# Kernel optimization log

Hardware: AMD Instinct MI355X
Metric: run time of the kernel (lower is better)

The kernel has to match this reference:

```python
import jax, jax.numpy as jnp
import numpy as np

N_INNER = 16
N_INPUT = 784
NET_DIM = 64
N_CAT = 256
NIP = 256


def fourier(x, coeff):
    # x: [N, in_features], coeff: [in_features, net_dim//2]
    xp = 2.0 * jnp.pi * (x @ coeff)
    # concat(cos, sin) then transpose -> [net_dim, N]
    return jnp.concatenate([jnp.cos(xp), jnp.sin(xp)], axis=-1).T


def setup_inputs() -> dict:
    key = jax.random.key(0)
    ks = jax.random.split(key, 8)
    s = 0.05  # conv weight scale (~kaiming-uniform magnitude)
    z = jax.random.normal(ks[0], (NIP,), jnp.float32)
    log_w = jax.random.normal(ks[1], (NIP,), jnp.float32)
    inner_coeff = jax.random.normal(ks[2], (2, NET_DIM // 2), jnp.float32)  # sigma=1.0
    inner_w1 = jax.random.normal(ks[3], (N_INNER * NET_DIM, NET_DIM), jnp.float32) * s
    inner_w2 = jax.random.normal(ks[4], (N_INNER, NET_DIM), jnp.float32) * s
    input_coeff = jax.random.normal(ks[5], (1, NET_DIM // 2), jnp.float32)
    input_w1 = jax.random.normal(ks[6], (N_INPUT * NET_DIM, NET_DIM), jnp.float32) * s
    input_w2 = jax.random.normal(ks[7], (N_INPUT, N_CAT, NET_DIM), jnp.float32) * s
    return {"z": z, "log_w": log_w, "inner_coeff": inner_coeff,
            "inner_w1": inner_w1, "inner_w2": inner_w2,
            "input_coeff": input_coeff, "input_w1": input_w1,
            "input_w2": input_w2, "n_chunks": 1}


def reference(z, log_w, inner_coeff, inner_w1, inner_w2, input_coeff, input_w1, input_w2, n_chunks):
    nip = z.shape[0]
    # all-pairs grid: [nip^2, 2] (repeat_interleave, repeat)
    z2d = jnp.stack([jnp.repeat(z, nip), jnp.tile(z, nip)], axis=-1)
    # inner net (quad mode forces first conv groups=1 -> dense matmul)
    ff = fourier(z2d, inner_coeff)                 # [net_dim, nip^2]
    h = jnp.tanh(inner_w1 @ ff)                    # [N_INNER*net_dim, nip^2]
    h = h.reshape(N_INNER, NET_DIM, nip * nip)
    logits = -jax.nn.softplus(jnp.einsum('gd,gdn->gn', inner_w2, h))
    logits = logits.reshape(N_INNER, nip, nip)
    log_inner = logits - jax.nn.logsumexp(logits + log_w, axis=-1, keepdims=True) + log_w
    inner_param = jnp.swapaxes(jnp.exp(log_inner), -1, -2)   # [N_INNER, nip, nip]
    # input net
    ffi = fourier(z[:, None], input_coeff)         # [net_dim, nip]
    hi = jnp.tanh(input_w1 @ ffi).reshape(N_INPUT, NET_DIM, nip)
    in_logits = jnp.einsum('gcd,gdn->gcn', input_w2, hi)     # [N_INPUT, N_CAT, nip]
    input_param = jax.nn.log_softmax(jnp.swapaxes(in_logits, 1, 2), axis=-1)  # [N_INPUT, nip, N_CAT]
    return inner_param, input_param
```

## Files before the change

kernel.cpp:

```cpp
#include <hip/hip_runtime.h>

typedef unsigned short ushort_t;
typedef float f32x4 __attribute__((ext_vector_type(4)));
typedef __bf16 bf16x8 __attribute__((ext_vector_type(8)));

#define PI2 6.283185307179586f

__device__ inline float bf2f(ushort_t u){
  union { unsigned int i; float f; } x; x.i = ((unsigned int)u) << 16; return x.f;
}
__device__ inline float fast_tanh(float x){
  float e = __expf(2.0f*x);
  return 1.0f - 2.0f/(e + 1.0f);
}

__global__ __launch_bounds__(256, 4) void inner_kernel(
    const float* __restrict__ z,
    const float* __restrict__ log_w,
    const float* __restrict__ icoef,
    const float* __restrict__ w1,
    const float* __restrict__ w2,
    float* __restrict__ out0)
{
  const int tx   = threadIdx.x;
  const int lane = tx & 63, wid = tx >> 6;
  const int i    = blockIdx.x >> 2;
  const int gq   = blockIdx.x & 3;

  __shared__ __bf16 sh_ffB[16 * 2 * 64 * 8];
  __shared__ float  sredw[4][256];
  __shared__ float  sred4[4];

  const float zi = z[i];
  const float zj = z[tx];
  const float lw = log_w[tx];

  {
    const int t = tx >> 4, n = tx & 15;
    #pragma unroll
    for (int q = 0; q < 4; q++){
      union { __bf16 h[8]; uint4 v; } pc, ps;
      #pragma unroll
      for (int ii = 0; ii < 8; ii++){
        int k = 8*q + ii;
        float xp = PI2 * (zi*icoef[k] + zj*icoef[32+k]);
        float sv, cv;
        __sincosf(xp, &sv, &cv);
        pc.h[ii] = (__bf16)cv;
        ps.h[ii] = (__bf16)sv;
      }
      ((uint4*)sh_ffB)[(t*2+0)*64 + 16*q + n] = pc.v;
      ((uint4*)sh_ffB)[(t*2+1)*64 + 16*q + n] = ps.v;
    }
  }
  __syncthreads();

  const int w = wid;
  #pragma unroll 1
  for (int gg = 0; gg < 4; gg++){
    const int g = gq*4 + gg;

    const float* Ar = w1 + (size_t)(g*64 + 16*w + (lane&15))*64 + (lane>>4)*8;
    bf16x8 A0, A1;
    #pragma unroll
    for (int ii = 0; ii < 8; ii++){
      A0[ii] = (__bf16)Ar[ii];
      A1[ii] = (__bf16)Ar[32+ii];
    }
    const float4 w2v = *(const float4*)(w2 + g*64 + 16*w + 4*(lane>>4));

    float part[16];
    #pragma unroll 4
    for (int t = 0; t < 16; t++){
      bf16x8 B0 = *(const bf16x8*)(sh_ffB + ((size_t)(t*2+0)*64 + lane)*8);
      bf16x8 B1 = *(const bf16x8*)(sh_ffB + ((size_t)(t*2+1)*64 + lane)*8);
      f32x4 acc = {0.f, 0.f, 0.f, 0.f};
      acc = __builtin_amdgcn_mfma_f32_16x16x32_bf16(A0, B0, acc, 0, 0, 0);
      acc = __builtin_amdgcn_mfma_f32_16x16x32_bf16(A1, B1, acc, 0, 0, 0);
      float p = 0.f;
      p = fmaf(w2v.x, fast_tanh(acc[0]), p);
      p = fmaf(w2v.y, fast_tanh(acc[1]), p);
      p = fmaf(w2v.z, fast_tanh(acc[2]), p);
      p = fmaf(w2v.w, fast_tanh(acc[3]), p);
      part[t] = p;
    }
    #pragma unroll
    for (int t = 0; t < 16; t++){
      float p = part[t];
      p += __shfl_xor(p, 16, 64);
      p += __shfl_xor(p, 32, 64);
      if ((lane >> 4) == 0) sredw[w][t*16 + lane] = p;
    }
    __syncthreads();

    float y = sredw[0][tx] + sredw[1][tx] + sredw[2][tx] + sredw[3][tx];
    float sp = fmaxf(y, 0.f) + __logf(1.f + __expf(-fabsf(y)));
    float tval = -sp + lw;
    float m = tval;
    #pragma unroll
    for (int o = 32; o > 0; o >>= 1) m = fmaxf(m, __shfl_xor(m, o, 64));
    if (lane == 0) sred4[wid] = m;
    __syncthreads();
    m = fmaxf(fmaxf(sred4[0], sred4[1]), fmaxf(sred4[2], sred4[3]));
    __syncthreads();
    float e = __expf(tval - m);
    float s = e;
    #pragma unroll
    for (int o = 32; o > 0; o >>= 1) s += __shfl_xor(s, o, 64);
    if (lane == 0) sred4[wid] = s;
    __syncthreads();
    s = sred4[0] + sred4[1] + sred4[2] + sred4[3];
    float lse = m + __logf(s);
    out0[(size_t)g*65536 + (size_t)tx*256 + i] = __expf(tval - lse);
    __syncthreads();
  }
}

__global__ __launch_bounds__(256, 3) void input_kernel(
    const float* __restrict__ z,
    const float* __restrict__ ipc,
    const float* __restrict__ w1,
    const float* __restrict__ w2,
    float* __restrict__ out1)
{
  const int tx   = threadIdx.x;
  const int lane = tx & 63, wid = tx >> 6;
  const int b    = blockIdx.x;
  const int xcd  = b & 7;
  const int s    = b >> 3;
  const int g    = xcd*98 + (s >> 2);
  const int nt   = s & 3;

  __shared__ __bf16 sh_fB[4 * 2 * 64 * 8];
  __shared__ __bf16 sh_hB[4 * 2 * 64 * 8];
  __shared__ ushort_t sh_lg[64 * 260];
  __shared__ float sm[4][64], ssv[4][64], slse[64];

  {
    const int n = tx & 63, q = tx >> 6;
    const int t = n >> 4, nn = n & 15;
    const float zn = z[nt*64 + n];
    union { __bf16 h[8]; uint4 v; } pc, ps;
    #pragma unroll
    for (int ii = 0; ii < 8; ii++){
      float xp = PI2 * zn * ipc[8*q + ii];
      float sv, cv;
      __sincosf(xp, &sv, &cv);
      pc.h[ii] = (__bf16)cv;
      ps.h[ii] = (__bf16)sv;
    }
    ((uint4*)sh_fB)[(t*2+0)*64 + 16*q + nn] = pc.v;
    ((uint4*)sh_fB)[(t*2+1)*64 + 16*q + nn] = ps.v;
  }
  __syncthreads();

  {
    const int w = wid;
    const float* Ar = w1 + (size_t)g*4096 + (size_t)(16*w + (lane&15))*64 + (lane>>4)*8;
    bf16x8 A0, A1;
    #pragma unroll
    for (int ii = 0; ii < 8; ii++){
      A0[ii] = (__bf16)Ar[ii];
      A1[ii] = (__bf16)Ar[32+ii];
    }
    const int q2 = lane >> 4, nn = lane & 15;
    const int dlt = w >> 1;
    #pragma unroll
    for (int t = 0; t < 4; t++){
      bf16x8 B0 = *(const bf16x8*)(sh_fB + ((size_t)(t*2+0)*64 + lane)*8);
      bf16x8 B1 = *(const bf16x8*)(sh_fB + ((size_t)(t*2+1)*64 + lane)*8);
      f32x4 acc = {0.f, 0.f, 0.f, 0.f};
      acc = __builtin_amdgcn_mfma_f32_16x16x32_bf16(A0, B0, acc, 0, 0, 0);
      acc = __builtin_amdgcn_mfma_f32_16x16x32_bf16(A1, B1, acc, 0, 0, 0);
      #pragma unroll
      for (int r = 0; r < 4; r++){
        int d  = 16*w + 4*q2 + r;
        int qB = (d & 31) >> 3, iB = d & 7;
        sh_hB[((size_t)(t*2+dlt)*64 + qB*16 + nn)*8 + iB] = (__bf16)fast_tanh(acc[r]);
      }
    }
  }
  __syncthreads();

  {
    const int w = wid;
    const float* w2g = w2 + (size_t)g*16384;
    #pragma unroll 1
    for (int cc = 0; cc < 4; cc++){
      const int ct = 4*w + cc;
      const float* Ar = w2g + (size_t)(16*ct + (lane&15))*64 + (lane>>4)*8;
      bf16x8 A0, A1;
      #pragma unroll
      for (int ii = 0; ii < 8; ii++){
        A0[ii] = (__bf16)Ar[ii];
        A1[ii] = (__bf16)Ar[32+ii];
      }
      #pragma unroll
      for (int t = 0; t < 4; t++){
        bf16x8 B0 = *(const bf16x8*)(sh_hB + ((size_t)(t*2+0)*64 + lane)*8);
        bf16x8 B1 = *(const bf16x8*)(sh_hB + ((size_t)(t*2+1)*64 + lane)*8);
        f32x4 acc = {0.f, 0.f, 0.f, 0.f};
        acc = __builtin_amdgcn_mfma_f32_16x16x32_bf16(A0, B0, acc, 0, 0, 0);
        acc = __builtin_amdgcn_mfma_f32_16x16x32_bf16(A1, B1, acc, 0, 0, 0);
        int c0 = 16*ct + 4*(lane>>4);
        int nn = 16*t + (lane&15);
        union { ushort_t u[4]; uint2 v; } pk;
        #pragma unroll
        for (int r = 0; r < 4; r++){
          union { float f; unsigned int i; } x; x.f = acc[r];
          unsigned int rr = x.i + 0x7fffu + ((x.i >> 16) & 1u);
          pk.u[r] = (ushort_t)(rr >> 16);
        }
        *(uint2*)(sh_lg + (size_t)nn*260 + c0) = pk.v;
      }
    }
  }
  __syncthreads();

  {
    const int n = tx & 63, cq = tx >> 6;
    const ushort_t* row = sh_lg + (size_t)n*260 + cq*64;
    float m = -3.0e38f;
    #pragma unroll 4
    for (int ci = 0; ci < 64; ci++) m = fmaxf(m, bf2f(row[ci]));
    float s = 0.f;
    #pragma unroll 4
    for (int ci = 0; ci < 64; ci++) s += __expf(bf2f(row[ci]) - m);
    sm[cq][n] = m; ssv[cq][n] = s;
  }
  __syncthreads();
  if (tx < 64){
    float M = fmaxf(fmaxf(sm[0][tx], sm[1][tx]), fmaxf(sm[2][tx], sm[3][tx]));
    float S = ssv[0][tx]*__expf(sm[0][tx]-M) + ssv[1][tx]*__expf(sm[1][tx]-M)
            + ssv[2][tx]*__expf(sm[2][tx]-M) + ssv[3][tx]*__expf(sm[3][tx]-M);
    slse[tx] = M + __logf(S);
  }
  __syncthreads();
  {
    size_t base = (size_t)g*65536 + (size_t)nt*64*256;
    #pragma unroll 1
    for (int rr = 0; rr < 64; rr++){
      out1[base + (size_t)rr*256 + tx] = bf2f(sh_lg[(size_t)rr*260 + tx]) - slse[rr];
    }
  }
}

extern "C" void kernel_launch(void* const* d_in, const int* in_sizes, int n_in,
                              void* d_out, int out_size, void* d_ws, size_t ws_size,
                              hipStream_t stream)
{
  const float* z     = (const float*)d_in[0];
  const float* lw    = (const float*)d_in[1];
  const float* icoef = (const float*)d_in[2];
  const float* iw1   = (const float*)d_in[3];
  const float* iw2   = (const float*)d_in[4];
  const float* ipc   = (const float*)d_in[5];
  const float* inw1  = (const float*)d_in[6];
  const float* inw2  = (const float*)d_in[7];

  float* out0 = (float*)d_out;
  float* out1 = out0 + (size_t)16*256*256;

  hipLaunchKernelGGL(inner_kernel, dim3(1024), dim3(256), 0, stream, z, lw, icoef, iw1, iw2, out0);
  hipLaunchKernelGGL(input_kernel, dim3(3136), dim3(256), 0, stream, z, ipc, inw1, inw2, out1);
}
```

Measured before the change: 358.1 us.

## Fuse inner and input kernels into one launch with register-resident logits

Merges the two kernels into one grid in which the first 256 blocks handle the inner net and the rest handle the input net. The inner path now computes Fourier features on the fly per tile, keeps all four weight tiles in registers, does a per-row softmax with a shared-memory buffer, and writes coalesced float4 stores. The input path keeps logits in fp32 registers rather than rounding them to bf16 in LDS, does the log-softmax through warp shuffles plus a small LDS reduction, and writes vectorized output. Weight loads are vectorized as float4. The aim is to remove a launch boundary, cut LDS traffic and uncoalesced stores, at the cost of higher register pressure.

```diff
diff --git a/kernel.cpp b/kernel.cpp
--- a/kernel.cpp
+++ b/kernel.cpp
@@ -5,242 +5,278 @@
 typedef __bf16 bf16x8 __attribute__((ext_vector_type(8)));
 
 #define PI2 6.283185307179586f
-
-__device__ inline float bf2f(ushort_t u){
-  union { unsigned int i; float f; } x; x.i = ((unsigned int)u) << 16; return x.f;
-}
+#define N_INNER_BLOCKS 256
+#define N_INPUT_BLOCKS 3136
+
 __device__ inline float fast_tanh(float x){
   float e = __expf(2.0f*x);
   return 1.0f - 2.0f/(e + 1.0f);
 }
 
-__global__ __launch_bounds__(256, 4) void inner_kernel(
+__global__ __launch_bounds__(256, 3) void fused_kernel(
     const float* __restrict__ z,
     const float* __restrict__ log_w,
     const float* __restrict__ icoef,
-    const float* __restrict__ w1,
-    const float* __restrict__ w2,
-    float* __restrict__ out0)
+    const float* __restrict__ iw1,
+    const float* __restrict__ iw2,
+    const float* __restrict__ ipc,
+    const float* __restrict__ nw1,
+    const float* __restrict__ nw2,
+    float* __restrict__ out0,
+    float* __restrict__ out1)
 {
+  __shared__ __align__(16) char smem[18688];
   const int tx   = threadIdx.x;
-  const int lane = tx & 63, wid = tx >> 6;
-  const int i    = blockIdx.x >> 2;
-  const int gq   = blockIdx.x & 3;
-
-  __shared__ __bf16 sh_ffB[16 * 2 * 64 * 8];
-  __shared__ float  sredw[4][256];
-  __shared__ float  sred4[4];
-
-  const float zi = z[i];
-  const float zj = z[tx];
-  const float lw = log_w[tx];
-
-  {
-    const int t = tx >> 4, n = tx & 15;
-    #pragma unroll
-    for (int q = 0; q < 4; q++){
+  const int lane = tx & 63, w = tx >> 6;
+  const int q    = lane >> 4, l15 = lane & 15;
+
+  if (blockIdx.x < N_INNER_BLOCKS){
+    const int ib = blockIdx.x;
+    const int g  = ib >> 4;
+    const int i0 = (ib & 15) << 4;
+
+    float* res = (float*)smem;
+    float* zz  = (float*)(smem + 16640);
+    float* lwv = (float*)(smem + 17664);
+
+    zz[tx]  = z[tx];
+    lwv[tx] = log_w[tx];
+    __syncthreads();
+
+    float cA[8], cB[8];
+    #pragma unroll
+    for (int ii = 0; ii < 8; ii++){
+      cA[ii] = PI2 * icoef[8*q + ii];
+      cB[ii] = PI2 * icoef[32 + 8*q + ii];
+    }
+
+    bf16x8 A0[4], A1[4];
+    #pragma unroll
+    for (int dt = 0; dt < 4; dt++){
+      const float* Ar = iw1 + (size_t)(g*64 + 16*dt + l15)*64 + 8*q;
+      f32x4 a0 = *(const f32x4*)Ar;
+      f32x4 a1 = *(const f32x4*)(Ar + 4);
+      f32x4 a2 = *(const f32x4*)(Ar + 32);
+      f32x4 a3 = *(const f32x4*)(Ar + 36);
+      #pragma unroll
+      for (int ii = 0; ii < 4; ii++){
+        A0[dt][ii]   = (__bf16)a0[ii];
+        A0[dt][4+ii] = (__bf16)a1[ii];
+        A1[dt][ii]   = (__bf16)a2[ii];
+        A1[dt][4+ii] = (__bf16)a3[ii];
+      }
+    }
+    f32x4 w2v[4];
+    #pragma unroll
+    for (int dt = 0; dt < 4; dt++)
+      w2v[dt] = *(const f32x4*)(iw2 + g*64 + 16*dt + 4*q);
+
+    #pragma unroll 1
+    for (int il = 0; il < 4; il++){
+      const int irow = 4*w + il;
+      const float zi = zz[i0 + irow];
+      float xA[8];
+      #pragma unroll
+      for (int ii = 0; ii < 8; ii++) xA[ii] = zi * cA[ii];
+
+      float m = -3.0e38f;
+      #pragma unroll 2
+      for (int jt = 0; jt < 16; jt++){
+        const float zj = zz[16*jt + l15];
+        bf16x8 B0, B1;
+        #pragma unroll
+        for (int ii = 0; ii < 8; ii++){
+          float sv, cv;
+          __sincosf(xA[ii] + zj*cB[ii], &sv, &cv);
+          B0[ii] = (__bf16)cv;
+          B1[ii] = (__bf16)sv;
+        }
+        float p = 0.f;
+        #pragma unroll
+        for (int dt = 0; dt < 4; dt++){
+          f32x4 acc = {0.f, 0.f, 0.f, 0.f};
+          acc = __builtin_amdgcn_mfma_f32_16x16x32_bf16(A0[dt], B0, acc, 0, 0, 0);
+          acc = __builtin_amdgcn_mfma_f32_16x16x32_bf16(A1[dt], B1, acc, 0, 0, 0);
+          p = fmaf(w2v[dt][0], fast_tanh(acc[0]), p);
+          p = fmaf(w2v[dt][1], fast_tanh(acc[1]), p);
+          p = fmaf(w2v[dt][2], fast_tanh(acc[2]), p);
+          p = fmaf(w2v[dt][3], fast_tanh(acc[3]), p);
+        }
+        p += __shfl_xor(p, 16, 64);
+        p += __shfl_xor(p, 32, 64);
+        float sp = fmaxf(p, 0.f) + __logf(1.f + __expf(-fabsf(p)));
+        float tval = -sp + lwv[16*jt + l15];
+        if (q == 0) res[irow*260 + 16*jt + l15] = tval;
+        m = fmaxf(m, tval);
+      }
+      #pragma unroll
+      for (int o = 1; o < 16; o <<= 1) m = fmaxf(m, __shfl_xor(m, o, 64));
+      float s = 0.f;
+      #pragma unroll
+      for (int jt = 0; jt < 16; jt++)
+        s += __expf(res[irow*260 + 16*jt + l15] - m);
+      #pragma unroll
+      for (int o = 1; o < 16; o <<= 1) s += __shfl_xor(s, o, 64);
+      const float lse = m + __logf(s);
+      if (q == 0){
+        #pragma unroll
+        for (int jt = 0; jt < 16; jt++){
+          const int idx = irow*260 + 16*jt + l15;
+          res[idx] = __expf(res[idx] - lse);
+        }
+      }
+    }
+    __syncthreads();
+    {
+      const int j2 = tx >> 2, c4 = tx & 3;
+      const size_t base = (size_t)g*65536 + (size_t)i0 + 4*c4;
+      #pragma unroll
+      for (int it2 = 0; it2 < 4; it2++){
+        const int j = 64*it2 + j2;
+        f32x4 v;
+        #pragma unroll
+        for (int rr = 0; rr < 4; rr++) v[rr] = res[(4*c4 + rr)*260 + j];
+        *(f32x4*)(out0 + base + (size_t)j*256) = v;
+      }
+    }
+  } else {
+    const int b   = blockIdx.x - N_INNER_BLOCKS;
+    const int xcd = b & 7;
+    const int s5  = b >> 3;
+    const int g   = xcd*98 + (s5 >> 2);
+    const int nt  = s5 & 3;
+
+    __bf16* fB   = (__bf16*)smem;
+    __bf16* hB   = (__bf16*)(smem + 8192);
+    float*  wred = (float*)(smem + 16384);
+    float*  sred = (float*)(smem + 17408);
+
+    {
+      const int n = tx & 63, qq = tx >> 6;
+      const int t = n >> 4, nn = n & 15;
+      const float zn = z[nt*64 + n];
       union { __bf16 h[8]; uint4 v; } pc, ps;
       #pragma unroll
       for (int ii = 0; ii < 8; ii++){
-        int k = 8*q + ii;
-        float xp = PI2 * (zi*icoef[k] + zj*icoef[32+k]);
         float sv, cv;
-        __sincosf(xp, &sv, &cv);
+        __sincosf(PI2 * zn * ipc[8*qq + ii], &sv, &cv);
         pc.h[ii] = (__bf16)cv;
         ps.h[ii] = (__bf16)sv;
       }
-      ((uint4*)sh_ffB)[(t*2+0)*64 + 16*q + n] = pc.v;
-      ((uint4*)sh_ffB)[(t*2+1)*64 + 16*q + n] = ps.v;
-    }
-  }
-  __syncthreads();
-
-  const int w = wid;
-  #pragma unroll 1
-  for (int gg = 0; gg < 4; gg++){
-    const int g = gq*4 + gg;
-
-    const float* Ar = w1 + (size_t)(g*64 + 16*w + (lane&15))*64 + (lane>>4)*8;
-    bf16x8 A0, A1;
-    #pragma unroll
-    for (int ii = 0; ii < 8; ii++){
-      A0[ii] = (__bf16)Ar[ii];
-      A1[ii] = (__bf16)Ar[32+ii];
-    }
-    const float4 w2v = *(const float4*)(w2 + g*64 + 16*w + 4*(lane>>4));
-
-    float part[16];
-    #pragma unroll 4
-    for (int t = 0; t < 16; t++){
-      bf16x8 B0 = *(const bf16x8*)(sh_ffB + ((size_t)(t*2+0)*64 + lane)*8);
-      bf16x8 B1 = *(const bf16x8*)(sh_ffB + ((size_t)(t*2+1)*64 + lane)*8);
-      f32x4 acc = {0.f, 0.f, 0.f, 0.f};
-      acc = __builtin_amdgcn_mfma_f32_16x16x32_bf16(A0, B0, acc, 0, 0, 0);
-      acc = __builtin_amdgcn_mfma_f32_16x16x32_bf16(A1, B1, acc, 0, 0, 0);
-      float p = 0.f;
-      p = fmaf(w2v.x, fast_tanh(acc[0]), p);
-      p = fmaf(w2v.y, fast_tanh(acc[1]), p);
-      p = fmaf(w2v.z, fast_tanh(acc[2]), p);
-      p = fmaf(w2v.w, fast_tanh(acc[3]), p);
-      part[t] = p;
-    }
-    #pragma unroll
-    for (int t = 0; t < 16; t++){
-      float p = part[t];
-      p += __shfl_xor(p, 16, 64);
-      p += __shfl_xor(p, 32, 64);
-      if ((lane >> 4) == 0) sredw[w][t*16 + lane] = p;
-    }
-    __syncthreads();
-
-    float y = sredw[0][tx] + sredw[1][tx] + sredw[2][tx] + sredw[3][tx];
-    float sp = fmaxf(y, 0.f) + __logf(1.f + __expf(-fabsf(y)));
-    float tval = -sp + lw;
-    float m = tval;
-    #pragma unroll
-    for (int o = 32; o > 0; o >>= 1) m = fmaxf(m, __shfl_xor(m, o, 64));
-    if (lane == 0) sred4[wid] = m;
-    __syncthreads();
-    m = fmaxf(fmaxf(sred4[0], sred4[1]), fmaxf(sred4[2], sred4[3]));
-    __syncthreads();
-    float e = __expf(tval - m);
-    float s = e;
-    #pragma unroll
-    for (int o = 32; o > 0; o >>= 1) s += __shfl_xor(s, o, 64);
-    if (lane == 0) sred4[wid] = s;
-    __syncthreads();
-    s = sred4[0] + sred4[1] + sred4[2] + sred4[3];
-    float lse = m + __logf(s);
-    out0[(size_t)g*65536 + (size_t)tx*256 + i] = __expf(tval - lse);
-    __syncthreads();
-  }
-}
-
-__global__ __launch_bounds__(256, 3) void input_kernel(
-    const float* __restrict__ z,
-    const float* __restrict__ ipc,
-    const float* __restrict__ w1,
-    const float* __restrict__ w2,
-    float* __restrict__ out1)
-{
-  const int tx   = threadIdx.x;
-  const int lane = tx & 63, wid = tx >> 6;
-  const int b    = blockIdx.x;
-  const int xcd  = b & 7;
-  const int s    = b >> 3;
-  const int g    = xcd*98 + (s >> 2);
-  const int nt   = s & 3;
-
-  __shared__ __bf16 sh_fB[4 * 2 * 64 * 8];
-  __shared__ __bf16 sh_hB[4 * 2 * 64 * 8];
-  __shared__ ushort_t sh_lg[64 * 260];
-  __shared__ float sm[4][64], ssv[4][64], slse[64];
-
-  {
-    const int n = tx & 63, q = tx >> 6;
-    const int t = n >> 4, nn = n & 15;
-    const float zn = z[nt*64 + n];
-    union { __bf16 h[8]; uint4 v; } pc, ps;
-    #pragma unroll
-    for (int ii = 0; ii < 8; ii++){
-      float xp = PI2 * zn * ipc[8*q + ii];
-      float sv, cv;
-      __sincosf(xp, &sv, &cv);
-      pc.h[ii] = (__bf16)cv;
-      ps.h[ii] = (__bf16)sv;
-    }
-    ((uint4*)sh_fB)[(t*2+0)*64 + 16*q + nn] = pc.v;
-    ((uint4*)sh_fB)[(t*2+1)*64 + 16*q + nn] = ps.v;
-  }
-  __syncthreads();
-
-  {
-    const int w = wid;
-    const float* Ar = w1 + (size_t)g*4096 + (size_t)(16*w + (lane&15))*64 + (lane>>4)*8;
-    bf16x8 A0, A1;
-    #pragma unroll
-    for (int ii = 0; ii < 8; ii++){
-      A0[ii] = (__bf16)Ar[ii];
-      A1[ii] = (__bf16)Ar[32+ii];
-    }
-    const int q2 = lane >> 4, nn = lane & 15;
-    const int dlt = w >> 1;
-    #pragma unroll
-    for (int t = 0; t < 4; t++){
-      bf16x8 B0 = *(const bf16x8*)(sh_fB + ((size_t)(t*2+0)*64 + lane)*8);
-      bf16x8 B1 = *(const bf16x8*)(sh_fB + ((size_t)(t*2+1)*64 + lane)*8);
-      f32x4 acc = {0.f, 0.f, 0.f, 0.f};
-      acc = __builtin_amdgcn_mfma_f32_16x16x32_bf16(A0, B0, acc, 0, 0, 0);
-      acc = __builtin_amdgcn_mfma_f32_16x16x32_bf16(A1, B1, acc, 0, 0, 0);
-      #pragma unroll
-      for (int r = 0; r < 4; r++){
-        int d  = 16*w + 4*q2 + r;
-        int qB = (d & 31) >> 3, iB = d & 7;
-        sh_hB[((size_t)(t*2+dlt)*64 + qB*16 + nn)*8 + iB] = (__bf16)fast_tanh(acc[r]);
-      }
-    }
-  }
-  __syncthreads();
-
-  {
-    const int w = wid;
-    const float* w2g = w2 + (size_t)g*16384;
-    #pragma unroll 1
-    for (int cc = 0; cc < 4; cc++){
-      const int ct = 4*w + cc;
-      const float* Ar = w2g + (size_t)(16*ct + (lane&15))*64 + (lane>>4)*8;
+      ((uint4*)fB)[(t*2+0)*64 + 16*qq + nn] = pc.v;
+      ((uint4*)fB)[(t*2+1)*64 + 16*qq + nn] = ps.v;
+    }
+    __syncthreads();
+
+    {
+      const float* Ar = nw1 + (size_t)g*4096 + (size_t)(16*w + l15)*64 + 8*q;
+      f32x4 a0 = *(const f32x4*)Ar;
+      f32x4 a1 = *(const f32x4*)(Ar + 4);
+      f32x4 a2 = *(const f32x4*)(Ar + 32);
+      f32x4 a3 = *(const f32x4*)(Ar + 36);
       bf16x8 A0, A1;
       #pragma unroll
-      for (int ii = 0; ii < 8; ii++){
-        A0[ii] = (__bf16)Ar[ii];
-        A1[ii] = (__bf16)Ar[32+ii];
-      }
+      for (int ii = 0; ii < 4; ii++){
+        A0[ii] = (__bf16)a0[ii];  A0[4+ii] = (__bf16)a1[ii];
+        A1[ii] = (__bf16)a2[ii];  A1[4+ii] = (__bf16)a3[ii];
+      }
+      const int dlt = w >> 1;
+      const int qB  = 2*(w & 1) + (q >> 1);
+      const int iB0 = 4*(q & 1);
       #pragma unroll
       for (int t = 0; t < 4; t++){
-        bf16x8 B0 = *(const bf16x8*)(sh_hB + ((size_t)(t*2+0)*64 + lane)*8);
-        bf16x8 B1 = *(const bf16x8*)(sh_hB + ((size_t)(t*2+1)*64 + lane)*8);
+        bf16x8 B0 = *(const bf16x8*)(fB + ((t*2+0)*64 + lane)*8);
+        bf16x8 B1 = *(const bf16x8*)(fB + ((t*2+1)*64 + lane)*8);
         f32x4 acc = {0.f, 0.f, 0.f, 0.f};
         acc = __builtin_amdgcn_mfma_f32_16x16x32_bf16(A0, B0, acc, 0, 0, 0);
         acc = __builtin_amdgcn_mfma_f32_16x16x32_bf16(A1, B1, acc, 0, 0, 0);
-        int c0 = 16*ct + 4*(lane>>4);
-        int nn = 16*t + (lane&15);
-        union { ushort_t u[4]; uint2 v; } pk;
-        #pragma unroll
-        for (int r = 0; r < 4; r++){
-          union { float f; unsigned int i; } x; x.f = acc[r];
-          unsigned int rr = x.i + 0x7fffu + ((x.i >> 16) & 1u);
-          pk.u[r] = (ushort_t)(rr >> 16);
-        }
-        *(uint2*)(sh_lg + (size_t)nn*260 + c0) = pk.v;
-      }
-    }
-  }
-  __syncthreads();
-
-  {
-    const int n = tx & 63, cq = tx >> 6;
-    const ushort_t* row = sh_lg + (size_t)n*260 + cq*64;
-    float m = -3.0e38f;
-    #pragma unroll 4
-    for (int ci = 0; ci < 64; ci++) m = fmaxf(m, bf2f(row[ci]));
-    float s = 0.f;
-    #pragma unroll 4
-    for (int ci = 0; ci < 64; ci++) s += __expf(bf2f(row[ci]) - m);
-    sm[cq][n] = m; ssv[cq][n] = s;
-  }
-  __syncthreads();
-  if (tx < 64){
-    float M = fmaxf(fmaxf(sm[0][tx], sm[1][tx]), fmaxf(sm[2][tx], sm[3][tx]));
-    float S = ssv[0][tx]*__expf(sm[0][tx]-M) + ssv[1][tx]*__expf(sm[1][tx]-M)
-            + ssv[2][tx]*__expf(sm[2][tx]-M) + ssv[3][tx]*__expf(sm[3][tx]-M);
-    slse[tx] = M + __logf(S);
-  }
-  __syncthreads();
-  {
-    size_t base = (size_t)g*65536 + (size_t)nt*64*256;
-    #pragma unroll 1
-    for (int rr = 0; rr < 64; rr++){
-      out1[base + (size_t)rr*256 + tx] = bf2f(sh_lg[(size_t)rr*260 + tx]) - slse[rr];
+        union { __bf16 h[4]; uint2 v; } pk;
+        #pragma unroll
+        for (int r = 0; r < 4; r++) pk.h[r] = (__bf16)fast_tanh(acc[r]);
+        *(uint2*)(hB + ((size_t)(t*2+dlt)*64 + qB*16 + l15)*8 + iB0) = pk.v;
+      }
+    }
+    __syncthreads();
+
+    float lg[4][4][4];
+    {
+      const float* w2g = nw2 + (size_t)g*16384;
+      #pragma unroll
+      for (int cc = 0; cc < 4; cc++){
+        const float* Ar = w2g + (size_t)(16*(4*w + cc) + l15)*64 + 8*q;
+        f32x4 a0 = *(const f32x4*)Ar;
+        f32x4 a1 = *(const f32x4*)(Ar + 4);
+        f32x4 a2 = *(const f32x4*)(Ar + 32);
+        f32x4 a3 = *(const f32x4*)(Ar + 36);
+        bf16x8 A0, A1;
+        #pragma unroll
+        for (int ii = 0; ii < 4; ii++){
+          A0[ii] = (__bf16)a0[ii];  A0[4+ii] = (__bf16)a1[ii];
+          A1[ii] = (__bf16)a2[ii];  A1[4+ii] = (__bf16)a3[ii];
+        }
+        #pragma unroll
+        for (int t = 0; t < 4; t++){
+          bf16x8 B0 = *(const bf16x8*)(hB + ((t*2+0)*64 + lane)*8);
+          bf16x8 B1 = *(const bf16x8*)(hB + ((t*2+1)*64 + lane)*8);
+          f32x4 acc = {0.f, 0.f, 0.f, 0.f};
+          acc = __builtin_amdgcn_mfma_f32_16x16x32_bf16(A0, B0, acc, 0, 0, 0);
+          acc = __builtin_amdgcn_mfma_f32_16x16x32_bf16(A1, B1, acc, 0, 0, 0);
+          #pragma unroll
+          for (int r = 0; r < 4; r++) lg[cc][t][r] = acc[r];
+        }
+      }
+    }
+
+    float lsev[4];
+    #pragma unroll
+    for (int t = 0; t < 4; t++){
+      float mt = lg[0][t][0];
+      #pragma unroll
+      for (int cc = 0; cc < 4; cc++){
+        #pragma unroll
+        for (int r = 0; r < 4; r++) mt = fmaxf(mt, lg[cc][t][r]);
+      }
+      mt = fmaxf(mt, __shfl_xor(mt, 16, 64));
+      mt = fmaxf(mt, __shfl_xor(mt, 32, 64));
+      if (q == 0) wred[w*64 + 16*t + l15] = mt;
+    }
+    __syncthreads();
+    #pragma unroll
+    for (int t = 0; t < 4; t++){
+      const int nn = 16*t + l15;
+      float M = fmaxf(fmaxf(wred[nn], wred[64+nn]), fmaxf(wred[128+nn], wred[192+nn]));
+      float st = 0.f;
+      #pragma unroll
+      for (int cc = 0; cc < 4; cc++){
+        #pragma unroll
+        for (int r = 0; r < 4; r++) st += __expf(lg[cc][t][r] - M);
+      }
+      st += __shfl_xor(st, 16, 64);
+      st += __shfl_xor(st, 32, 64);
+      if (q == 0) sred[w*64 + 16*t + l15] = st;
+      lsev[t] = M;
+    }
+    __syncthreads();
+    #pragma unroll
+    for (int t = 0; t < 4; t++){
+      const int nn = 16*t + l15;
+      float S = sred[nn] + sred[64+nn] + sred[128+nn] + sred[192+nn];
+      lsev[t] = lsev[t] + __logf(S);
+    }
+
+    {
+      const size_t base = (size_t)g*65536 + (size_t)(nt*64)*256 + (size_t)(64*w);
+      #pragma unroll
+      for (int t = 0; t < 4; t++){
+        const size_t rowb = base + (size_t)(16*t + l15)*256;
+        #pragma unroll
+        for (int cc = 0; cc < 4; cc++){
+          f32x4 v;
+          #pragma unroll
+          for (int r = 0; r < 4; r++) v[r] = lg[cc][t][r] - lsev[t];
+          *(f32x4*)(out1 + rowb + 16*cc + 4*q) = v;
+        }
+      }
     }
   }
 }
@@ -261,6 +297,6 @@
   float* out0 = (float*)d_out;
   float* out1 = out0 + (size_t)16*256*256;
 
-  hipLaunchKernelGGL(inner_kernel, dim3(1024), dim3(256), 0, stream, z, lw, icoef, iw1, iw2, out0);
-  hipLaunchKernelGGL(input_kernel, dim3(3136), dim3(256), 0, stream, z, ipc, inw1, inw2, out1);
+  hipLaunchKernelGGL(fused_kernel, dim3(N_INNER_BLOCKS + N_INPUT_BLOCKS), dim3(256), 0, stream,
+                     z, lw, icoef, iw1, iw2, ipc, inw1, inw2, out0, out1);
 }
```

Result: faster. 311.4 us (-13.0%).
